# Kernel tuning notes

Measured on AMD Instinct MI355X. Metric: run time of the kernel, lower is better.

Reference implementation:

```python
import jax, jax.numpy as jnp
import numpy as np

B, L, D_MODEL = 16, 512, 768
S, D_LLM = 2048, 4096
H = 8
E = D_MODEL // H  # d_keys = 96


def setup_inputs() -> dict:
    key = jax.random.key(0)
    ks = jax.random.split(key, 10)
    sc_dm = 1.0 / np.sqrt(D_MODEL)
    sc_dl = 1.0 / np.sqrt(D_LLM)
    return {
        "target": jax.random.normal(ks[0], (B, L, D_MODEL), jnp.float32),
        "source": jax.random.normal(ks[1], (S, D_LLM), jnp.float32),
        "Wq": jax.random.normal(ks[2], (D_MODEL, H * E), jnp.float32) * sc_dm,
        "bq": jnp.zeros((H * E,), jnp.float32),
        "Wk": jax.random.normal(ks[3], (D_LLM, H * E), jnp.float32) * sc_dl,
        "bk": jnp.zeros((H * E,), jnp.float32),
        "Wv": jax.random.normal(ks[4], (D_LLM, H * E), jnp.float32) * sc_dl,
        "bv": jnp.zeros((H * E,), jnp.float32),
        "Wo": jax.random.normal(ks[5], (H * E, D_LLM), jnp.float32) * sc_dm,
        "bo": jnp.zeros((D_LLM,), jnp.float32),
    }


def reference(target, source, Wq, bq, Wk, bk, Wv, bv, Wo, bo):
    # Q: (B, L, H, E); K, V: (S, H, E) -- K/V are shared across the batch.
    Q = (target @ Wq + bq).reshape(B, L, H, E)
    K = (source @ Wk + bk).reshape(S, H, E)
    V = (source @ Wv + bv).reshape(S, H, E)
    # scores: (B, H, L, S)
    scores = jnp.einsum('blhe,she->bhls', Q, K) / jnp.sqrt(jnp.asarray(E, Q.dtype))
    attn = jax.nn.softmax(scores, axis=-1)  # dropout is identity in eval mode
    rep = jnp.einsum('bhls,she->blhe', attn, V).reshape(B, L, H * E)
    return rep @ Wo + bo  # (B, L, d_llm)
```

## Files before the change

### kernel.cpp

```cpp
#include <hip/hip_runtime.h>
#include <hip/hip_bf16.h>
#include <stdint.h>

typedef __hip_bfloat16 bf16;
typedef __attribute__((ext_vector_type(8))) short short8;
typedef __attribute__((ext_vector_type(4))) float floatx4;

__device__ __forceinline__ void gll16(const bf16* g, const bf16* lds_base) {
  __builtin_amdgcn_global_load_lds(
      (const __attribute__((address_space(1))) unsigned int*)g,
      (__attribute__((address_space(3))) unsigned int*)lds_base,
      16, 0, 0);
}

__device__ __forceinline__ unsigned pk2(float a, float b) {
  union { __hip_bfloat16 h; unsigned short u; } ca, cb;
  ca.h = __float2bfloat16(a);
  cb.h = __float2bfloat16(b);
  return (unsigned)ca.u | ((unsigned)cb.u << 16);
}

__global__ __launch_bounds__(256) void cvt_both(const float* __restrict__ t_in,
                                                const float* __restrict__ s_in,
                                                bf16* __restrict__ t_out,
                                                bf16* __restrict__ s_out) {
  int bid = blockIdx.x;
  const float* in;
  bf16* out;
  int i;
  if (bid < 6144) {
    in = t_in; out = t_out; i = (bid * 256 + threadIdx.x) * 4;
  } else {
    in = s_in; out = s_out; i = ((bid - 6144) * 256 + threadIdx.x) * 4;
  }
  float4 v = *(const float4*)(in + i);
  out[i + 0] = __float2bfloat16(v.x);
  out[i + 1] = __float2bfloat16(v.y);
  out[i + 2] = __float2bfloat16(v.z);
  out[i + 3] = __float2bfloat16(v.w);
}

__global__ __launch_bounds__(256) void trans_all(const float* __restrict__ Wq,
                                                 const float* __restrict__ Wk,
                                                 const float* __restrict__ Wv,
                                                 const float* __restrict__ Wo,
                                                 bf16* __restrict__ WqT,
                                                 bf16* __restrict__ WkvT,
                                                 bf16* __restrict__ WoT) {
  __shared__ float t[32][33];
  int id = blockIdx.x;
  const float* in; bf16* out; int R, C, cx, ry;
  if (id < 576)        { in = Wq; out = WqT; R = 768;  C = 768;  id -= 0;    cx = id % 24;  ry = id / 24; }
  else if (id < 3648)  { in = Wk; out = WkvT; R = 4096; C = 768; id -= 576;  cx = id % 24;  ry = id / 24; }
  else if (id < 6720)  { in = Wv; out = WkvT + (size_t)768 * 4096; R = 4096; C = 768; id -= 3648; cx = id % 24; ry = id / 24; }
  else                 { in = Wo; out = WoT; R = 768;  C = 4096; id -= 6720; cx = id % 128; ry = id / 128; }
  int tx = threadIdx.x & 31, ty = threadIdx.x >> 5;
  int c0 = cx * 32, r0 = ry * 32;
#pragma unroll
  for (int j = 0; j < 4; ++j)
    t[ty + j * 8][tx] = in[(size_t)(r0 + ty + j * 8) * C + c0 + tx];
  __syncthreads();
#pragma unroll
  for (int j = 0; j < 4; ++j)
    out[(size_t)(c0 + ty + j * 8) * R + r0 + tx] = __float2bfloat16(t[tx][ty + j * 8]);
}

template <int BM, bool OUT_F32>
__global__ __launch_bounds__(256) void gemm_bt(const bf16* __restrict__ A,
                                               const bf16* __restrict__ BT,
                                               const float* __restrict__ bias,
                                               void* __restrict__ Cv,
                                               int M, int N, int K, int ldc) {
  __shared__ bf16 As[BM * 32];
  __shared__ bf16 Bs[128 * 32];
  const int tid = threadIdx.x;
  const int w = tid >> 6, lane = tid & 63;
  const int ln = lane & 15, quad = lane >> 4;
  const int wm = w >> 1, wn = w & 1;
  const int m0 = blockIdx.x * BM, n0 = blockIdx.y * 128;
  constexpr int MT = BM / 32;
  constexpr int TA = BM / 64;

  floatx4 acc[MT][4] = {};

  for (int k0 = 0; k0 < K; k0 += 32) {
    __syncthreads();
#pragma unroll
    for (int t = 0; t < TA; ++t) {
      int cidb = (w * TA + t) * 64;
      int cid = cidb + lane;
      int row = cid >> 2, ko = (cid & 3) * 8;
      gll16(A + (size_t)(m0 + row) * K + k0 + ko, As + cidb * 8);
    }
#pragma unroll
    for (int t = 0; t < 2; ++t) {
      int cidb = (w * 2 + t) * 64;
      int cid = cidb + lane;
      int row = cid >> 2, ko = (cid & 3) * 8;
      gll16(BT + (size_t)(n0 + row) * K + k0 + ko, Bs + cidb * 8);
    }
    __syncthreads();
    const short8* Av = (const short8*)As;
    const short8* Bv = (const short8*)Bs;
    short8 a[MT], b[4];
#pragma unroll
    for (int mt = 0; mt < MT; ++mt) a[mt] = Av[(wm * (BM / 2) + mt * 16 + ln) * 4 + quad];
#pragma unroll
    for (int nt = 0; nt < 4; ++nt) b[nt] = Bv[(wn * 64 + nt * 16 + ln) * 4 + quad];
#pragma unroll
    for (int mt = 0; mt < MT; ++mt)
#pragma unroll
      for (int nt = 0; nt < 4; ++nt)
        acc[mt][nt] = __builtin_amdgcn_mfma_f32_16x16x32_bf16(a[mt], b[nt], acc[mt][nt], 0, 0, 0);
  }

#pragma unroll
  for (int nt = 0; nt < 4; ++nt) {
    int n = n0 + wn * 64 + nt * 16 + ln;
    float bv_ = bias[n];
#pragma unroll
    for (int mt = 0; mt < MT; ++mt)
#pragma unroll
      for (int r = 0; r < 4; ++r) {
        int m = m0 + wm * (BM / 2) + mt * 16 + quad * 4 + r;
        float v = acc[mt][nt][r] + bv_;
        size_t idx = (size_t)m * ldc + n;
        if (OUT_F32)
          ((float*)Cv)[idx] = v;
        else
          ((bf16*)Cv)[idx] = __float2bfloat16(v);
      }
  }
}

template <int NS>
__global__ __launch_bounds__(256) void gemm_kv_splitk(const bf16* __restrict__ A,
                                                      const bf16* __restrict__ BT,
                                                      float* __restrict__ P) {
  __shared__ bf16 As[128 * 32];
  __shared__ bf16 Bs[128 * 32];
  const int tid = threadIdx.x;
  const int w = tid >> 6, lane = tid & 63;
  const int ln = lane & 15, quad = lane >> 4;
  const int wm = w >> 1, wn = w & 1;
  const int m0 = blockIdx.x * 128, n0 = blockIdx.y * 128;
  constexpr int KSEG = 4096 / NS;
  const int kbeg = blockIdx.z * KSEG;
  float* Pz = P + (size_t)blockIdx.z * 2048 * 1536;

  floatx4 acc[4][4] = {};

  for (int k0 = kbeg; k0 < kbeg + KSEG; k0 += 32) {
    __syncthreads();
#pragma unroll
    for (int t = 0; t < 2; ++t) {
      int cidb = (w * 2 + t) * 64;
      int cid = cidb + lane;
      int row = cid >> 2, ko = (cid & 3) * 8;
      gll16(A + (size_t)(m0 + row) * 4096 + k0 + ko, As + cidb * 8);
      gll16(BT + (size_t)(n0 + row) * 4096 + k0 + ko, Bs + cidb * 8);
    }
    __syncthreads();
    const short8* Av = (const short8*)As;
    const short8* Bv = (const short8*)Bs;
    short8 a[4], b[4];
#pragma unroll
    for (int mt = 0; mt < 4; ++mt) a[mt] = Av[(wm * 64 + mt * 16 + ln) * 4 + quad];
#pragma unroll
    for (int nt = 0; nt < 4; ++nt) b[nt] = Bv[(wn * 64 + nt * 16 + ln) * 4 + quad];
#pragma unroll
    for (int mt = 0; mt < 4; ++mt)
#pragma unroll
      for (int nt = 0; nt < 4; ++nt)
        acc[mt][nt] = __builtin_amdgcn_mfma_f32_16x16x32_bf16(a[mt], b[nt], acc[mt][nt], 0, 0, 0);
  }

#pragma unroll
  for (int nt = 0; nt < 4; ++nt) {
    int n = n0 + wn * 64 + nt * 16 + ln;
#pragma unroll
    for (int mt = 0; mt < 4; ++mt)
#pragma unroll
      for (int r = 0; r < 4; ++r) {
        int m = m0 + wm * 64 + mt * 16 + quad * 4 + r;
        Pz[(size_t)m * 1536 + n] = acc[mt][nt][r];
      }
  }
}

template <int NS>
__global__ __launch_bounds__(256) void reduce_kv_both(const float* __restrict__ P,
                                                      const float* __restrict__ bk,
                                                      const float* __restrict__ bv,
                                                      bf16* __restrict__ Kws,
                                                      bf16* __restrict__ VTws) {
  __shared__ float t[32][33];
  if (blockIdx.y == 0) {
    int idx = (blockIdx.x * 256 + threadIdx.x) * 4;
    int m = idx / 768, n = idx % 768;
    float4 acc = *(const float4*)(bk + n);
#pragma unroll
    for (int z = 0; z < NS; ++z) {
      float4 a = *(const float4*)(P + (size_t)z * 2048 * 1536 + (size_t)m * 1536 + n);
      acc.x += a.x; acc.y += a.y; acc.z += a.z; acc.w += a.w;
    }
    Kws[(size_t)m * 768 + n + 0] = __float2bfloat16(acc.x);
    Kws[(size_t)m * 768 + n + 1] = __float2bfloat16(acc.y);
    Kws[(size_t)m * 768 + n + 2] = __float2bfloat16(acc.z);
    Kws[(size_t)m * 768 + n + 3] = __float2bfloat16(acc.w);
  } else {
    int tx = threadIdx.x & 31, ty = threadIdx.x >> 5;
    int c0 = (blockIdx.x % 24) * 32;
    int r0 = (blockIdx.x / 24) * 32;
#pragma unroll
    for (int j = 0; j < 4; ++j) {
      size_t off = (size_t)(r0 + ty + j * 8) * 1536 + 768 + c0 + tx;
      float s = 0.f;
#pragma unroll
      for (int z = 0; z < NS; ++z) s += P[off + (size_t)z * 2048 * 1536];
      t[ty + j * 8][tx] = s;
    }
    __syncthreads();
#pragma unroll
    for (int j = 0; j < 4; ++j) {
      int e = c0 + ty + j * 8;
      VTws[(size_t)e * 2048 + r0 + tx] = __float2bfloat16(t[tx][ty + j * 8] + bv[e]);
    }
  }
}

__global__ __launch_bounds__(256, 4) void attn_kernel(const bf16* __restrict__ Q,
                                                      const bf16* __restrict__ Kt,
                                                      const bf16* __restrict__ VT,
                                                      bf16* __restrict__ rep) {
  __shared__ __align__(16) bf16 Ks[64 * 13 * 8];
  __shared__ __align__(16) bf16 Vs[96 * 9 * 8];
  __shared__ __align__(16) bf16 Ps[64 * 72];
  __shared__ float Rs[2][64];

  const int tid = threadIdx.x, w = tid >> 6, lane = tid & 63;
  const int ln = lane & 15, quad = lane >> 4;
  const int wq = w >> 1, ws = w & 1;
  const int h = blockIdx.x;
  const int yy = blockIdx.y;
  const int b = yy >> 3, qt = yy & 7;

  const bf16* Qg = Q + (size_t)(b * 512 + qt * 64) * 768 + h * 96;
  short8 qf[2][3];
#pragma unroll
  for (int mt = 0; mt < 2; ++mt)
#pragma unroll
    for (int es = 0; es < 3; ++es)
      qf[mt][es] = *(const short8*)(Qg + (size_t)(wq * 32 + mt * 16 + ln) * 768 + (es * 4 + quad) * 8);

  const bf16* Kgh = Kt + h * 96;
  const bf16* Vgh = VT + (size_t)h * 96 * 2048;

  int krow[3], koff[3], vrow[3], voff[3];
#pragma unroll
  for (int t = 0; t < 3; ++t) {
    int cid = t * 256 + tid;
    krow[t] = cid / 12; koff[t] = cid % 12;
    vrow[t] = cid >> 3; voff[t] = cid & 7;
  }

  short8 kreg[3], vreg[3];
#pragma unroll
  for (int t = 0; t < 3; ++t) {
    kreg[t] = *(const short8*)(Kgh + (size_t)krow[t] * 768 + koff[t] * 8);
    vreg[t] = *(const short8*)(Vgh + (size_t)vrow[t] * 2048 + voff[t] * 8);
  }

  floatx4 po[2][3] = {};
  float psum[2] = {};
  const float cexp = 1.4426950408889634f / 9.797958971132712f;

  for (int it = 0; it < 32; ++it) {
    const int s0 = it * 64;
    __syncthreads();

#pragma unroll
    for (int t = 0; t < 3; ++t) {
      *(short8*)(&Ks[(krow[t] * 13 + koff[t]) * 8]) = kreg[t];
      *(short8*)(&Vs[(vrow[t] * 9 + voff[t]) * 8]) = vreg[t];
    }
    if (it < 31) {
#pragma unroll
      for (int t = 0; t < 3; ++t) {
        kreg[t] = *(const short8*)(Kgh + (size_t)(s0 + 64 + krow[t]) * 768 + koff[t] * 8);
        vreg[t] = *(const short8*)(Vgh + (size_t)vrow[t] * 2048 + s0 + 64 + voff[t] * 8);
      }
    }
    __syncthreads();

    floatx4 sacc[2][2] = {};
    const short8* Kv = (const short8*)Ks;
#pragma unroll
    for (int es = 0; es < 3; ++es) {
      short8 kf[2];
#pragma unroll
      for (int ct = 0; ct < 2; ++ct) kf[ct] = Kv[(ws * 32 + ct * 16 + ln) * 13 + es * 4 + quad];
#pragma unroll
      for (int mt = 0; mt < 2; ++mt)
#pragma unroll
        for (int ct = 0; ct < 2; ++ct)
          sacc[mt][ct] = __builtin_amdgcn_mfma_f32_16x16x32_bf16(kf[ct], qf[mt][es], sacc[mt][ct], 0, 0, 0);
    }

#pragma unroll
    for (int mt = 0; mt < 2; ++mt) {
      float rs = 0.f;
#pragma unroll
      for (int ct = 0; ct < 2; ++ct) {
        float p0 = exp2f(sacc[mt][ct][0] * cexp);
        float p1 = exp2f(sacc[mt][ct][1] * cexp);
        float p2 = exp2f(sacc[mt][ct][2] * cexp);
        float p3 = exp2f(sacc[mt][ct][3] * cexp);
        rs += (p0 + p1) + (p2 + p3);
        uint2 uu;
        uu.x = pk2(p0, p1);
        uu.y = pk2(p2, p3);
        *(uint2*)(Ps + (wq * 32 + mt * 16 + ln) * 72 + ws * 32 + ct * 16 + quad * 4) = uu;
      }
      psum[mt] += rs;
    }
    __syncthreads();

    const short8* Pv = (const short8*)Ps;
    const short8* Vv = (const short8*)Vs;
#pragma unroll
    for (int ks = 0; ks < 2; ++ks) {
      short8 pa[2];
#pragma unroll
      for (int mt = 0; mt < 2; ++mt) pa[mt] = Pv[(wq * 32 + mt * 16 + ln) * 9 + ks * 4 + quad];
#pragma unroll
      for (int nt = 0; nt < 3; ++nt) {
        short8 vb = Vv[(ws * 48 + nt * 16 + ln) * 9 + ks * 4 + quad];
#pragma unroll
        for (int mt = 0; mt < 2; ++mt)
          po[mt][nt] = __builtin_amdgcn_mfma_f32_16x16x32_bf16(pa[mt], vb, po[mt][nt], 0, 0, 0);
      }
    }
  }

  float t0 = psum[0], t1 = psum[1];
  t0 += __shfl_xor(t0, 16, 64); t0 += __shfl_xor(t0, 32, 64);
  t1 += __shfl_xor(t1, 16, 64); t1 += __shfl_xor(t1, 32, 64);
  if (lane < 16) {
    Rs[ws][wq * 32 + lane] = t0;
    Rs[ws][wq * 32 + 16 + lane] = t1;
  }
  __syncthreads();

  float linv[2][4];
#pragma unroll
  for (int mt = 0; mt < 2; ++mt)
#pragma unroll
    for (int r = 0; r < 4; ++r) {
      int q = wq * 32 + mt * 16 + quad * 4 + r;
      float v = Rs[0][q] + Rs[1][q];
      linv[mt][r] = 1.f / fmaxf(v, 1e-37f);
    }

  bf16* og = rep + (size_t)(b * 512 + qt * 64) * 768 + h * 96;
#pragma unroll
  for (int mt = 0; mt < 2; ++mt)
#pragma unroll
    for (int nt = 0; nt < 3; ++nt)
#pragma unroll
      for (int r = 0; r < 4; ++r) {
        int row = wq * 32 + mt * 16 + quad * 4 + r;
        int e = ws * 48 + nt * 16 + ln;
        og[(size_t)row * 768 + e] = __float2bfloat16(po[mt][nt][r] * linv[mt][r]);
      }
}

extern "C" void kernel_launch(void* const* d_in, const int* in_sizes, int n_in,
                              void* d_out, int out_size, void* d_ws, size_t ws_size,
                              hipStream_t stream) {
  const float* target = (const float*)d_in[0];
  const float* source = (const float*)d_in[1];
  const float* Wq = (const float*)d_in[2];
  const float* bq = (const float*)d_in[3];
  const float* Wk = (const float*)d_in[4];
  const float* bk = (const float*)d_in[5];
  const float* Wv = (const float*)d_in[6];
  const float* bv = (const float*)d_in[7];
  const float* Wo = (const float*)d_in[8];
  const float* bo = (const float*)d_in[9];
  float* out = (float*)d_out;

  bf16* ws = (bf16*)d_ws;
  bf16* tgt_bf = ws;
  bf16* src_bf = tgt_bf + 6291456;
  bf16* WqT = src_bf + 8388608;
  bf16* WkvT = WqT + 589824;
  bf16* WoT = WkvT + 6291456;
  bf16* Qws = WoT + 3145728;
  bf16* Kws = Qws + 6291456;
  bf16* VTws = Kws + 1572864;
  float* Pkv = (float*)(ws + 34144256);
  const size_t PKV_SEG = 2048ull * 1536 * 4;
  const size_t NEED2 = 68288512ull + 2 * PKV_SEG;
  const size_t NEED4 = 68288512ull + 4 * PKV_SEG;
  bf16* repws = src_bf;

  cvt_both<<<14336, 256, 0, stream>>>(target, source, tgt_bf, src_bf);
  trans_all<<<9792, 256, 0, stream>>>(Wq, Wk, Wv, Wo, WqT, WkvT, WoT);

  gemm_bt<64, false><<<dim3(128, 6), 256, 0, stream>>>(tgt_bf, WqT, bq, Qws, 8192, 768, 768, 768);

  if (ws_size >= NEED4) {
    gemm_kv_splitk<4><<<dim3(16, 12, 4), 256, 0, stream>>>(src_bf, WkvT, Pkv);
    reduce_kv_both<4><<<dim3(1536, 2), 256, 0, stream>>>(Pkv, bk, bv, Kws, VTws);
  } else if (ws_size >= NEED2) {
    gemm_kv_splitk<2><<<dim3(16, 12, 2), 256, 0, stream>>>(src_bf, WkvT, Pkv);
    reduce_kv_both<2><<<dim3(1536, 2), 256, 0, stream>>>(Pkv, bk, bv, Kws, VTws);
  } else {
    gemm_bt<128, false><<<dim3(16, 6), 256, 0, stream>>>(src_bf, WkvT, bk, Kws, 2048, 768, 4096, 768);
    gemm_bt<128, false><<<dim3(16, 6), 256, 0, stream>>>(src_bf, WkvT + (size_t)768 * 4096, bv, Kws, 2048, 768, 4096, 768);
  }

  attn_kernel<<<dim3(8, 128), 256, 0, stream>>>(Qws, Kws, VTws, repws);

  gemm_bt<128, true><<<dim3(64, 32), 256, 0, stream>>>(repws, WoT, bo, out, 8192, 4096, 768, 4096);
}
```

Measured before the change: 473.8 us.

## Fuse fp32-to-bf16 input conversion into Q and KV GEMM loaders

Drops the standalone conversion kernel for target and source. The Q projection GEMM and the split-K KV GEMM now read fp32 activations directly, pack them to bf16 in registers and store them to LDS, which avoids writing and rereading bf16 copies. The KV GEMM M tile shrinks from 128 to 64 to raise block count. Split-K is capped at 2, with a split-1 plus reduce fallback, and the workspace layout is reorganised. The tradeoff is that A loads become synchronous register loads instead of direct global-to-LDS loads, and the A tile is loaded twice as often relative to B.

```diff
diff --git a/kernel.cpp b/kernel.cpp
--- a/kernel.cpp
+++ b/kernel.cpp
@@ -18,26 +18,6 @@
   ca.h = __float2bfloat16(a);
   cb.h = __float2bfloat16(b);
   return (unsigned)ca.u | ((unsigned)cb.u << 16);
-}
-
-__global__ __launch_bounds__(256) void cvt_both(const float* __restrict__ t_in,
-                                                const float* __restrict__ s_in,
-                                                bf16* __restrict__ t_out,
-                                                bf16* __restrict__ s_out) {
-  int bid = blockIdx.x;
-  const float* in;
-  bf16* out;
-  int i;
-  if (bid < 6144) {
-    in = t_in; out = t_out; i = (bid * 256 + threadIdx.x) * 4;
-  } else {
-    in = s_in; out = s_out; i = ((bid - 6144) * 256 + threadIdx.x) * 4;
-  }
-  float4 v = *(const float4*)(in + i);
-  out[i + 0] = __float2bfloat16(v.x);
-  out[i + 1] = __float2bfloat16(v.y);
-  out[i + 2] = __float2bfloat16(v.z);
-  out[i + 3] = __float2bfloat16(v.w);
 }
 
 __global__ __launch_bounds__(256) void trans_all(const float* __restrict__ Wq,
@@ -65,8 +45,8 @@
     out[(size_t)(c0 + ty + j * 8) * R + r0 + tx] = __float2bfloat16(t[tx][ty + j * 8]);
 }
 
-template <int BM, bool OUT_F32>
-__global__ __launch_bounds__(256) void gemm_bt(const bf16* __restrict__ A,
+template <int BM, bool OUT_F32, bool A_F32>
+__global__ __launch_bounds__(256) void gemm_bt(const void* __restrict__ Ain,
                                                const bf16* __restrict__ BT,
                                                const float* __restrict__ bias,
                                                void* __restrict__ Cv,
@@ -86,18 +66,37 @@
   for (int k0 = 0; k0 < K; k0 += 32) {
     __syncthreads();
 #pragma unroll
-    for (int t = 0; t < TA; ++t) {
-      int cidb = (w * TA + t) * 64;
-      int cid = cidb + lane;
-      int row = cid >> 2, ko = (cid & 3) * 8;
-      gll16(A + (size_t)(m0 + row) * K + k0 + ko, As + cidb * 8);
-    }
-#pragma unroll
     for (int t = 0; t < 2; ++t) {
       int cidb = (w * 2 + t) * 64;
       int cid = cidb + lane;
       int row = cid >> 2, ko = (cid & 3) * 8;
       gll16(BT + (size_t)(n0 + row) * K + k0 + ko, Bs + cidb * 8);
+    }
+    if constexpr (A_F32) {
+      const float* Af = (const float*)Ain;
+#pragma unroll
+      for (int t = 0; t < TA; ++t) {
+        int cid = t * 256 + tid;
+        int row = cid >> 2, ko = (cid & 3) * 8;
+        const float* ap = Af + (size_t)(m0 + row) * K + k0 + ko;
+        float4 f0 = *(const float4*)ap;
+        float4 f1 = *(const float4*)(ap + 4);
+        uint4 uu;
+        uu.x = pk2(f0.x, f0.y);
+        uu.y = pk2(f0.z, f0.w);
+        uu.z = pk2(f1.x, f1.y);
+        uu.w = pk2(f1.z, f1.w);
+        *(uint4*)(As + (size_t)cid * 8) = uu;
+      }
+    } else {
+      const bf16* Ab = (const bf16*)Ain;
+#pragma unroll
+      for (int t = 0; t < TA; ++t) {
+        int cidb = (w * TA + t) * 64;
+        int cid = cidb + lane;
+        int row = cid >> 2, ko = (cid & 3) * 8;
+        gll16(Ab + (size_t)(m0 + row) * K + k0 + ko, As + cidb * 8);
+      }
     }
     __syncthreads();
     const short8* Av = (const short8*)As;
@@ -134,21 +133,21 @@
 }
 
 template <int NS>
-__global__ __launch_bounds__(256) void gemm_kv_splitk(const bf16* __restrict__ A,
+__global__ __launch_bounds__(256) void gemm_kv_splitk(const float* __restrict__ A,
                                                       const bf16* __restrict__ BT,
                                                       float* __restrict__ P) {
-  __shared__ bf16 As[128 * 32];
+  __shared__ bf16 As[64 * 32];
   __shared__ bf16 Bs[128 * 32];
   const int tid = threadIdx.x;
   const int w = tid >> 6, lane = tid & 63;
   const int ln = lane & 15, quad = lane >> 4;
   const int wm = w >> 1, wn = w & 1;
-  const int m0 = blockIdx.x * 128, n0 = blockIdx.y * 128;
+  const int m0 = blockIdx.x * 64, n0 = blockIdx.y * 128;
   constexpr int KSEG = 4096 / NS;
   const int kbeg = blockIdx.z * KSEG;
   float* Pz = P + (size_t)blockIdx.z * 2048 * 1536;
 
-  floatx4 acc[4][4] = {};
+  floatx4 acc[2][4] = {};
 
   for (int k0 = kbeg; k0 < kbeg + KSEG; k0 += 32) {
     __syncthreads();
@@ -157,19 +156,30 @@
       int cidb = (w * 2 + t) * 64;
       int cid = cidb + lane;
       int row = cid >> 2, ko = (cid & 3) * 8;
-      gll16(A + (size_t)(m0 + row) * 4096 + k0 + ko, As + cidb * 8);
       gll16(BT + (size_t)(n0 + row) * 4096 + k0 + ko, Bs + cidb * 8);
+    }
+    {
+      int row = tid >> 2, ko = (tid & 3) * 8;
+      const float* ap = A + (size_t)(m0 + row) * 4096 + k0 + ko;
+      float4 f0 = *(const float4*)ap;
+      float4 f1 = *(const float4*)(ap + 4);
+      uint4 uu;
+      uu.x = pk2(f0.x, f0.y);
+      uu.y = pk2(f0.z, f0.w);
+      uu.z = pk2(f1.x, f1.y);
+      uu.w = pk2(f1.z, f1.w);
+      *(uint4*)(As + (size_t)tid * 8) = uu;
     }
     __syncthreads();
     const short8* Av = (const short8*)As;
     const short8* Bv = (const short8*)Bs;
-    short8 a[4], b[4];
-#pragma unroll
-    for (int mt = 0; mt < 4; ++mt) a[mt] = Av[(wm * 64 + mt * 16 + ln) * 4 + quad];
+    short8 a[2], b[4];
+#pragma unroll
+    for (int mt = 0; mt < 2; ++mt) a[mt] = Av[(wm * 32 + mt * 16 + ln) * 4 + quad];
 #pragma unroll
     for (int nt = 0; nt < 4; ++nt) b[nt] = Bv[(wn * 64 + nt * 16 + ln) * 4 + quad];
 #pragma unroll
-    for (int mt = 0; mt < 4; ++mt)
+    for (int mt = 0; mt < 2; ++mt)
 #pragma unroll
       for (int nt = 0; nt < 4; ++nt)
         acc[mt][nt] = __builtin_amdgcn_mfma_f32_16x16x32_bf16(a[mt], b[nt], acc[mt][nt], 0, 0, 0);
@@ -179,10 +189,10 @@
   for (int nt = 0; nt < 4; ++nt) {
     int n = n0 + wn * 64 + nt * 16 + ln;
 #pragma unroll
-    for (int mt = 0; mt < 4; ++mt)
+    for (int mt = 0; mt < 2; ++mt)
 #pragma unroll
       for (int r = 0; r < 4; ++r) {
-        int m = m0 + wm * 64 + mt * 16 + quad * 4 + r;
+        int m = m0 + wm * 32 + mt * 16 + quad * 4 + r;
         Pz[(size_t)m * 1536 + n] = acc[mt][nt][r];
       }
   }
@@ -391,37 +401,31 @@
   float* out = (float*)d_out;
 
   bf16* ws = (bf16*)d_ws;
-  bf16* tgt_bf = ws;
-  bf16* src_bf = tgt_bf + 6291456;
-  bf16* WqT = src_bf + 8388608;
+  bf16* WqT = ws;
   bf16* WkvT = WqT + 589824;
   bf16* WoT = WkvT + 6291456;
   bf16* Qws = WoT + 3145728;
   bf16* Kws = Qws + 6291456;
   bf16* VTws = Kws + 1572864;
-  float* Pkv = (float*)(ws + 34144256);
-  const size_t PKV_SEG = 2048ull * 1536 * 4;
-  const size_t NEED2 = 68288512ull + 2 * PKV_SEG;
-  const size_t NEED4 = 68288512ull + 4 * PKV_SEG;
-  bf16* repws = src_bf;
-
-  cvt_both<<<14336, 256, 0, stream>>>(target, source, tgt_bf, src_bf);
+  bf16* repws = VTws + 1572864;
+  float* Pkv = (float*)(repws + 6291456);
+  const size_t PKV_OFF = 25755648ull * 2;
+  const size_t SEG = 2048ull * 1536 * 4;
+  const size_t NEED2 = PKV_OFF + 2 * SEG;
+
   trans_all<<<9792, 256, 0, stream>>>(Wq, Wk, Wv, Wo, WqT, WkvT, WoT);
 
-  gemm_bt<64, false><<<dim3(128, 6), 256, 0, stream>>>(tgt_bf, WqT, bq, Qws, 8192, 768, 768, 768);
-
-  if (ws_size >= NEED4) {
-    gemm_kv_splitk<4><<<dim3(16, 12, 4), 256, 0, stream>>>(src_bf, WkvT, Pkv);
-    reduce_kv_both<4><<<dim3(1536, 2), 256, 0, stream>>>(Pkv, bk, bv, Kws, VTws);
-  } else if (ws_size >= NEED2) {
-    gemm_kv_splitk<2><<<dim3(16, 12, 2), 256, 0, stream>>>(src_bf, WkvT, Pkv);
+  gemm_bt<64, false, true><<<dim3(128, 6), 256, 0, stream>>>(target, WqT, bq, Qws, 8192, 768, 768, 768);
+
+  if (ws_size >= NEED2) {
+    gemm_kv_splitk<2><<<dim3(32, 12, 2), 256, 0, stream>>>(source, WkvT, Pkv);
     reduce_kv_both<2><<<dim3(1536, 2), 256, 0, stream>>>(Pkv, bk, bv, Kws, VTws);
   } else {
-    gemm_bt<128, false><<<dim3(16, 6), 256, 0, stream>>>(src_bf, WkvT, bk, Kws, 2048, 768, 4096, 768);
-    gemm_bt<128, false><<<dim3(16, 6), 256, 0, stream>>>(src_bf, WkvT + (size_t)768 * 4096, bv, Kws, 2048, 768, 4096, 768);
+    gemm_kv_splitk<1><<<dim3(32, 12, 1), 256, 0, stream>>>(source, WkvT, Pkv);
+    reduce_kv_both<1><<<dim3(1536, 2), 256, 0, stream>>>(Pkv, bk, bv, Kws, VTws);
   }
 
   attn_kernel<<<dim3(8, 128), 256, 0, stream>>>(Qws, Kws, VTws, repws);
 
-  gemm_bt<128, true><<<dim3(64, 32), 256, 0, stream>>>(repws, WoT, bo, out, 8192, 4096, 768, 4096);
-}
+  gemm_bt<128, true, false><<<dim3(64, 32), 256, 0, stream>>>(repws, WoT, bo, out, 8192, 4096, 768, 4096);
+}
```

Result: slower. 488.4 us (+3.1%).

## Merge conversion kernels and Q/KV projections into single launches, swizzle Wo GEMM

Applied to the files above, without the earlier changes.

Combines the input-cast and weight-transpose kernels into one launch, and fuses the Q projection with a split-K KV projection (now 64-row tiles, split 2) into one grid so both share the GPU. The output projection gets a dedicated kernel that remaps block IDs to group tiles for better L2 reuse of A/B panels. The intent is to cut launch count, fill the device better during the small Q GEMM, and improve cache locality in the large final GEMM. The split-4 path is dropped in favour of split-2 with smaller M tiles, which changes the per-block arithmetic intensity.

```diff
diff --git a/kernel.cpp b/kernel.cpp
--- a/kernel.cpp
+++ b/kernel.cpp
@@ -20,35 +20,33 @@
   return (unsigned)ca.u | ((unsigned)cb.u << 16);
 }
 
-__global__ __launch_bounds__(256) void cvt_both(const float* __restrict__ t_in,
-                                                const float* __restrict__ s_in,
-                                                bf16* __restrict__ t_out,
-                                                bf16* __restrict__ s_out) {
-  int bid = blockIdx.x;
-  const float* in;
-  bf16* out;
-  int i;
-  if (bid < 6144) {
-    in = t_in; out = t_out; i = (bid * 256 + threadIdx.x) * 4;
-  } else {
-    in = s_in; out = s_out; i = ((bid - 6144) * 256 + threadIdx.x) * 4;
-  }
-  float4 v = *(const float4*)(in + i);
-  out[i + 0] = __float2bfloat16(v.x);
-  out[i + 1] = __float2bfloat16(v.y);
-  out[i + 2] = __float2bfloat16(v.z);
-  out[i + 3] = __float2bfloat16(v.w);
-}
-
-__global__ __launch_bounds__(256) void trans_all(const float* __restrict__ Wq,
+__global__ __launch_bounds__(256) void cvt_trans(const float* __restrict__ t_in,
+                                                 const float* __restrict__ s_in,
+                                                 const float* __restrict__ Wq,
                                                  const float* __restrict__ Wk,
                                                  const float* __restrict__ Wv,
                                                  const float* __restrict__ Wo,
+                                                 bf16* __restrict__ t_out,
+                                                 bf16* __restrict__ s_out,
                                                  bf16* __restrict__ WqT,
                                                  bf16* __restrict__ WkvT,
                                                  bf16* __restrict__ WoT) {
   __shared__ float t[32][33];
-  int id = blockIdx.x;
+  int bid = blockIdx.x;
+  if (bid < 14336) {
+    const float* in;
+    bf16* out;
+    int i;
+    if (bid < 6144) { in = t_in; out = t_out; i = (bid * 256 + threadIdx.x) * 4; }
+    else            { in = s_in; out = s_out; i = ((bid - 6144) * 256 + threadIdx.x) * 4; }
+    float4 v = *(const float4*)(in + i);
+    out[i + 0] = __float2bfloat16(v.x);
+    out[i + 1] = __float2bfloat16(v.y);
+    out[i + 2] = __float2bfloat16(v.z);
+    out[i + 3] = __float2bfloat16(v.w);
+    return;
+  }
+  int id = bid - 14336;
   const float* in; bf16* out; int R, C, cx, ry;
   if (id < 576)        { in = Wq; out = WqT; R = 768;  C = 768;  id -= 0;    cx = id % 24;  ry = id / 24; }
   else if (id < 3648)  { in = Wk; out = WkvT; R = 4096; C = 768; id -= 576;  cx = id % 24;  ry = id / 24; }
@@ -65,126 +63,101 @@
     out[(size_t)(c0 + ty + j * 8) * R + r0 + tx] = __float2bfloat16(t[tx][ty + j * 8]);
 }
 
-template <int BM, bool OUT_F32>
-__global__ __launch_bounds__(256) void gemm_bt(const bf16* __restrict__ A,
-                                               const bf16* __restrict__ BT,
-                                               const float* __restrict__ bias,
-                                               void* __restrict__ Cv,
-                                               int M, int N, int K, int ldc) {
-  __shared__ bf16 As[BM * 32];
+__device__ __forceinline__ void gemm64_core(const bf16* __restrict__ A,
+                                            const bf16* __restrict__ BT,
+                                            int K, int kbeg, int kend,
+                                            int m0, int n0,
+                                            bf16* As, bf16* Bs,
+                                            floatx4 acc[2][4]) {
+  const int tid = threadIdx.x;
+  const int w = tid >> 6, lane = tid & 63;
+  const int ln = lane & 15, quad = lane >> 4;
+  for (int k0 = kbeg; k0 < kend; k0 += 32) {
+    __syncthreads();
+#pragma unroll
+    for (int t = 0; t < 2; ++t) {
+      int cidb = (w * 2 + t) * 64;
+      int cid = cidb + lane;
+      int row = cid >> 2, ko = (cid & 3) * 8;
+      gll16(BT + (size_t)(n0 + row) * K + k0 + ko, Bs + cidb * 8);
+    }
+    {
+      int cidb = w * 64;
+      int cid = cidb + lane;
+      int row = cid >> 2, ko = (cid & 3) * 8;
+      gll16(A + (size_t)(m0 + row) * K + k0 + ko, As + cidb * 8);
+    }
+    __syncthreads();
+    const short8* Av = (const short8*)As;
+    const short8* Bv = (const short8*)Bs;
+    const int wm = w >> 1, wn = w & 1;
+    short8 a[2], b[4];
+#pragma unroll
+    for (int mt = 0; mt < 2; ++mt) a[mt] = Av[(wm * 32 + mt * 16 + ln) * 4 + quad];
+#pragma unroll
+    for (int nt = 0; nt < 4; ++nt) b[nt] = Bv[(wn * 64 + nt * 16 + ln) * 4 + quad];
+#pragma unroll
+    for (int mt = 0; mt < 2; ++mt)
+#pragma unroll
+      for (int nt = 0; nt < 4; ++nt)
+        acc[mt][nt] = __builtin_amdgcn_mfma_f32_16x16x32_bf16(a[mt], b[nt], acc[mt][nt], 0, 0, 0);
+  }
+}
+
+template <int NS>
+__global__ __launch_bounds__(256) void qkv_proj(const bf16* __restrict__ tgt,
+                                                const bf16* __restrict__ src,
+                                                const bf16* __restrict__ WqT,
+                                                const bf16* __restrict__ WkvT,
+                                                const float* __restrict__ bq,
+                                                bf16* __restrict__ Qws,
+                                                float* __restrict__ P) {
+  __shared__ bf16 As[64 * 32];
   __shared__ bf16 Bs[128 * 32];
   const int tid = threadIdx.x;
   const int w = tid >> 6, lane = tid & 63;
   const int ln = lane & 15, quad = lane >> 4;
   const int wm = w >> 1, wn = w & 1;
-  const int m0 = blockIdx.x * BM, n0 = blockIdx.y * 128;
-  constexpr int MT = BM / 32;
-  constexpr int TA = BM / 64;
-
-  floatx4 acc[MT][4] = {};
-
-  for (int k0 = 0; k0 < K; k0 += 32) {
-    __syncthreads();
-#pragma unroll
-    for (int t = 0; t < TA; ++t) {
-      int cidb = (w * TA + t) * 64;
-      int cid = cidb + lane;
-      int row = cid >> 2, ko = (cid & 3) * 8;
-      gll16(A + (size_t)(m0 + row) * K + k0 + ko, As + cidb * 8);
-    }
-#pragma unroll
-    for (int t = 0; t < 2; ++t) {
-      int cidb = (w * 2 + t) * 64;
-      int cid = cidb + lane;
-      int row = cid >> 2, ko = (cid & 3) * 8;
-      gll16(BT + (size_t)(n0 + row) * K + k0 + ko, Bs + cidb * 8);
-    }
-    __syncthreads();
-    const short8* Av = (const short8*)As;
-    const short8* Bv = (const short8*)Bs;
-    short8 a[MT], b[4];
-#pragma unroll
-    for (int mt = 0; mt < MT; ++mt) a[mt] = Av[(wm * (BM / 2) + mt * 16 + ln) * 4 + quad];
-#pragma unroll
-    for (int nt = 0; nt < 4; ++nt) b[nt] = Bv[(wn * 64 + nt * 16 + ln) * 4 + quad];
-#pragma unroll
-    for (int mt = 0; mt < MT; ++mt)
-#pragma unroll
-      for (int nt = 0; nt < 4; ++nt)
-        acc[mt][nt] = __builtin_amdgcn_mfma_f32_16x16x32_bf16(a[mt], b[nt], acc[mt][nt], 0, 0, 0);
-  }
-
-#pragma unroll
-  for (int nt = 0; nt < 4; ++nt) {
-    int n = n0 + wn * 64 + nt * 16 + ln;
-    float bv_ = bias[n];
-#pragma unroll
-    for (int mt = 0; mt < MT; ++mt)
-#pragma unroll
-      for (int r = 0; r < 4; ++r) {
-        int m = m0 + wm * (BM / 2) + mt * 16 + quad * 4 + r;
-        float v = acc[mt][nt][r] + bv_;
-        size_t idx = (size_t)m * ldc + n;
-        if (OUT_F32)
-          ((float*)Cv)[idx] = v;
-        else
-          ((bf16*)Cv)[idx] = __float2bfloat16(v);
-      }
-  }
-}
-
-template <int NS>
-__global__ __launch_bounds__(256) void gemm_kv_splitk(const bf16* __restrict__ A,
-                                                      const bf16* __restrict__ BT,
-                                                      float* __restrict__ P) {
-  __shared__ bf16 As[128 * 32];
-  __shared__ bf16 Bs[128 * 32];
-  const int tid = threadIdx.x;
-  const int w = tid >> 6, lane = tid & 63;
-  const int ln = lane & 15, quad = lane >> 4;
-  const int wm = w >> 1, wn = w & 1;
-  const int m0 = blockIdx.x * 128, n0 = blockIdx.y * 128;
-  constexpr int KSEG = 4096 / NS;
-  const int kbeg = blockIdx.z * KSEG;
-  float* Pz = P + (size_t)blockIdx.z * 2048 * 1536;
-
-  floatx4 acc[4][4] = {};
-
-  for (int k0 = kbeg; k0 < kbeg + KSEG; k0 += 32) {
-    __syncthreads();
-#pragma unroll
-    for (int t = 0; t < 2; ++t) {
-      int cidb = (w * 2 + t) * 64;
-      int cid = cidb + lane;
-      int row = cid >> 2, ko = (cid & 3) * 8;
-      gll16(A + (size_t)(m0 + row) * 4096 + k0 + ko, As + cidb * 8);
-      gll16(BT + (size_t)(n0 + row) * 4096 + k0 + ko, Bs + cidb * 8);
-    }
-    __syncthreads();
-    const short8* Av = (const short8*)As;
-    const short8* Bv = (const short8*)Bs;
-    short8 a[4], b[4];
-#pragma unroll
-    for (int mt = 0; mt < 4; ++mt) a[mt] = Av[(wm * 64 + mt * 16 + ln) * 4 + quad];
-#pragma unroll
-    for (int nt = 0; nt < 4; ++nt) b[nt] = Bv[(wn * 64 + nt * 16 + ln) * 4 + quad];
-#pragma unroll
-    for (int mt = 0; mt < 4; ++mt)
-#pragma unroll
-      for (int nt = 0; nt < 4; ++nt)
-        acc[mt][nt] = __builtin_amdgcn_mfma_f32_16x16x32_bf16(a[mt], b[nt], acc[mt][nt], 0, 0, 0);
-  }
-
-#pragma unroll
-  for (int nt = 0; nt < 4; ++nt) {
-    int n = n0 + wn * 64 + nt * 16 + ln;
-#pragma unroll
-    for (int mt = 0; mt < 4; ++mt)
-#pragma unroll
-      for (int r = 0; r < 4; ++r) {
-        int m = m0 + wm * 64 + mt * 16 + quad * 4 + r;
-        Pz[(size_t)m * 1536 + n] = acc[mt][nt][r];
-      }
+  const int id = blockIdx.x;
+
+  floatx4 acc[2][4] = {};
+
+  if (id < 768) {
+    const int mb = id & 127, nb = id >> 7;
+    const int m0 = mb * 64, n0 = nb * 128;
+    gemm64_core(tgt, WqT, 768, 0, 768, m0, n0, As, Bs, acc);
+#pragma unroll
+    for (int nt = 0; nt < 4; ++nt) {
+      int n = n0 + wn * 64 + nt * 16 + ln;
+      float bv_ = bq[n];
+#pragma unroll
+      for (int mt = 0; mt < 2; ++mt)
+#pragma unroll
+        for (int r = 0; r < 4; ++r) {
+          int m = m0 + wm * 32 + mt * 16 + quad * 4 + r;
+          Qws[(size_t)m * 768 + n] = __float2bfloat16(acc[mt][nt][r] + bv_);
+        }
+    }
+  } else {
+    const int t2 = id - 768;
+    const int z = t2 / 384, r2 = t2 % 384;
+    const int mb = r2 & 31, nb = r2 >> 5;
+    const int m0 = mb * 64, n0 = nb * 128;
+    constexpr int KSEG = 4096 / NS;
+    const int kbeg = z * KSEG;
+    float* Pz = P + (size_t)z * 2048 * 1536;
+    gemm64_core(src, WkvT, 4096, kbeg, kbeg + KSEG, m0, n0, As, Bs, acc);
+#pragma unroll
+    for (int nt = 0; nt < 4; ++nt) {
+      int n = n0 + wn * 64 + nt * 16 + ln;
+#pragma unroll
+      for (int mt = 0; mt < 2; ++mt)
+#pragma unroll
+        for (int r = 0; r < 4; ++r) {
+          int m = m0 + wm * 32 + mt * 16 + quad * 4 + r;
+          Pz[(size_t)m * 1536 + n] = acc[mt][nt][r];
+        }
+    }
   }
 }
 
@@ -226,6 +199,63 @@
       int e = c0 + ty + j * 8;
       VTws[(size_t)e * 2048 + r0 + tx] = __float2bfloat16(t[tx][ty + j * 8] + bv[e]);
     }
+  }
+}
+
+__global__ __launch_bounds__(256) void gemm_wo(const bf16* __restrict__ A,
+                                               const bf16* __restrict__ BT,
+                                               const float* __restrict__ bias,
+                                               float* __restrict__ C) {
+  __shared__ bf16 As[128 * 32];
+  __shared__ bf16 Bs[128 * 32];
+  const int tid = threadIdx.x;
+  const int w = tid >> 6, lane = tid & 63;
+  const int ln = lane & 15, quad = lane >> 4;
+  const int wm = w >> 1, wn = w & 1;
+  const int W = blockIdx.x;
+  const int cid2 = (W & 7) * 256 + (W >> 3);
+  const int bx = cid2 >> 5, by = cid2 & 31;
+  const int m0 = bx * 128, n0 = by * 128;
+  const int K = 768, ldc = 4096;
+
+  floatx4 acc[4][4] = {};
+
+  for (int k0 = 0; k0 < K; k0 += 32) {
+    __syncthreads();
+#pragma unroll
+    for (int t = 0; t < 2; ++t) {
+      int cidb = (w * 2 + t) * 64;
+      int cid = cidb + lane;
+      int row = cid >> 2, ko = (cid & 3) * 8;
+      gll16(A + (size_t)(m0 + row) * K + k0 + ko, As + cidb * 8);
+      gll16(BT + (size_t)(n0 + row) * K + k0 + ko, Bs + cidb * 8);
+    }
+    __syncthreads();
+    const short8* Av = (const short8*)As;
+    const short8* Bv = (const short8*)Bs;
+    short8 a[4], b[4];
+#pragma unroll
+    for (int mt = 0; mt < 4; ++mt) a[mt] = Av[(wm * 64 + mt * 16 + ln) * 4 + quad];
+#pragma unroll
+    for (int nt = 0; nt < 4; ++nt) b[nt] = Bv[(wn * 64 + nt * 16 + ln) * 4 + quad];
+#pragma unroll
+    for (int mt = 0; mt < 4; ++mt)
+#pragma unroll
+      for (int nt = 0; nt < 4; ++nt)
+        acc[mt][nt] = __builtin_amdgcn_mfma_f32_16x16x32_bf16(a[mt], b[nt], acc[mt][nt], 0, 0, 0);
+  }
+
+#pragma unroll
+  for (int nt = 0; nt < 4; ++nt) {
+    int n = n0 + wn * 64 + nt * 16 + ln;
+    float bv_ = bias[n];
+#pragma unroll
+    for (int mt = 0; mt < 4; ++mt)
+#pragma unroll
+      for (int r = 0; r < 4; ++r) {
+        int m = m0 + wm * 64 + mt * 16 + quad * 4 + r;
+        C[(size_t)m * ldc + n] = acc[mt][nt][r] + bv_;
+      }
   }
 }
 
@@ -400,28 +430,22 @@
   bf16* Kws = Qws + 6291456;
   bf16* VTws = Kws + 1572864;
   float* Pkv = (float*)(ws + 34144256);
-  const size_t PKV_SEG = 2048ull * 1536 * 4;
-  const size_t NEED2 = 68288512ull + 2 * PKV_SEG;
-  const size_t NEED4 = 68288512ull + 4 * PKV_SEG;
+  const size_t SEG = 2048ull * 1536 * 4;
+  const size_t NEED2 = 68288512ull + 2 * SEG;
   bf16* repws = src_bf;
 
-  cvt_both<<<14336, 256, 0, stream>>>(target, source, tgt_bf, src_bf);
-  trans_all<<<9792, 256, 0, stream>>>(Wq, Wk, Wv, Wo, WqT, WkvT, WoT);
-
-  gemm_bt<64, false><<<dim3(128, 6), 256, 0, stream>>>(tgt_bf, WqT, bq, Qws, 8192, 768, 768, 768);
-
-  if (ws_size >= NEED4) {
-    gemm_kv_splitk<4><<<dim3(16, 12, 4), 256, 0, stream>>>(src_bf, WkvT, Pkv);
-    reduce_kv_both<4><<<dim3(1536, 2), 256, 0, stream>>>(Pkv, bk, bv, Kws, VTws);
-  } else if (ws_size >= NEED2) {
-    gemm_kv_splitk<2><<<dim3(16, 12, 2), 256, 0, stream>>>(src_bf, WkvT, Pkv);
+  cvt_trans<<<24128, 256, 0, stream>>>(target, source, Wq, Wk, Wv, Wo,
+                                       tgt_bf, src_bf, WqT, WkvT, WoT);
+
+  if (ws_size >= NEED2) {
+    qkv_proj<2><<<768 + 768, 256, 0, stream>>>(tgt_bf, src_bf, WqT, WkvT, bq, Qws, Pkv);
     reduce_kv_both<2><<<dim3(1536, 2), 256, 0, stream>>>(Pkv, bk, bv, Kws, VTws);
   } else {
-    gemm_bt<128, false><<<dim3(16, 6), 256, 0, stream>>>(src_bf, WkvT, bk, Kws, 2048, 768, 4096, 768);
-    gemm_bt<128, false><<<dim3(16, 6), 256, 0, stream>>>(src_bf, WkvT + (size_t)768 * 4096, bv, Kws, 2048, 768, 4096, 768);
+    qkv_proj<1><<<768 + 384, 256, 0, stream>>>(tgt_bf, src_bf, WqT, WkvT, bq, Qws, Pkv);
+    reduce_kv_both<1><<<dim3(1536, 2), 256, 0, stream>>>(Pkv, bk, bv, Kws, VTws);
   }
 
   attn_kernel<<<dim3(8, 128), 256, 0, stream>>>(Qws, Kws, VTws, repws);
 
-  gemm_bt<128, true><<<dim3(64, 32), 256, 0, stream>>>(repws, WoT, bo, out, 8192, 4096, 768, 4096);
-}
+  gemm_wo<<<2048, 256, 0, stream>>>(repws, WoT, bo, out);
+}
```

New measurement: 473.0 us. About the same (-0.2%).
